# Optimization experiments

Hardware: AMD Instinct MI355X
Metric: run time of the kernel (lower is better)

The kernel has to match this reference:

```python
import jax, jax.numpy as jnp
import numpy as np

N = 2048          # target nodes
N_NODES = 2048    # neighbor pool
D_IN = 256
D_EDGE = 16
D_HID = 32
D_OUT = 256


def _mlp(h, w1, b1, w2, b2):
    # Linear -> Tanh -> Linear
    return jnp.tanh(h @ w1 + b1) @ w2 + b2


def setup_inputs() -> dict:
    key = jax.random.key(0)
    ks = jax.random.split(key, 20)
    s = 0.05
    inp = {
        "x": jax.random.normal(ks[0], (N, D_IN), jnp.float32),
        "neibs": jax.random.normal(ks[1], (N_NODES, D_IN), jnp.float32),
        "edge_emb": jax.random.normal(ks[2], (N * N_NODES, D_EDGE), jnp.float32),
        # multiplicative binary mask (float, as in original ws * mask)
        "mask": (jax.random.uniform(ks[3], (N, N_NODES)) < 0.7).astype(jnp.float32),
        "ax_w1": jax.random.normal(ks[4], (D_IN, D_HID), jnp.float32) * s,
        "ax_b1": jnp.zeros((D_HID,), jnp.float32),
        "ax_w2": jax.random.normal(ks[5], (D_HID, D_HID), jnp.float32) * s,
        "ax_b2": jnp.zeros((D_HID,), jnp.float32),
        "an_w1": jax.random.normal(ks[6], (D_IN, D_HID), jnp.float32) * s,
        "an_b1": jnp.zeros((D_HID,), jnp.float32),
        "an_w2": jax.random.normal(ks[7], (D_HID, D_HID), jnp.float32) * s,
        "an_b2": jnp.zeros((D_HID,), jnp.float32),
        "ae_w1": jax.random.normal(ks[8], (D_EDGE, D_HID), jnp.float32) * s,
        "ae_b1": jnp.zeros((D_HID,), jnp.float32),
        "ae_w2": jax.random.normal(ks[9], (D_HID, D_HID), jnp.float32) * s,
        "ae_b2": jnp.zeros((D_HID,), jnp.float32),
        "fcx_w": jax.random.normal(ks[10], (2 * D_IN, D_OUT), jnp.float32) * s,
        "fcx_b": jnp.zeros((D_OUT,), jnp.float32),
    }
    return inp


def reference(x, neibs, edge_emb, mask,
              ax_w1, ax_b1, ax_w2, ax_b2,
              an_w1, an_b1, an_w2, an_b2,
              ae_w1, ae_b1, ae_w2, ae_b2,
              fcx_w, fcx_b):
    x_att = _mlp(x, ax_w1, ax_b1, ax_w2, ax_b2)          # (N, H)
    neib_att = _mlp(neibs, an_w1, an_b1, an_w2, an_b2)   # (n_nodes, H)
    # edge attention is computed in the original forward but never used (dead code)
    _edge_att = _mlp(edge_emb, ae_w1, ae_b1, ae_w2, ae_b2)
    # multiplicative masking (NOT additive -inf), then softmax over neighbors
    ws = jnp.einsum('nh,mh->nm', x_att, neib_att) * mask  # (N, n_nodes)
    ws = jax.nn.softmax(ws, axis=1)
    agg_neib = jax.nn.sigmoid(ws @ neibs)                 # (N, D_IN)
    # concat_node=False path: concat -> fc_x -> sigmoid; dropout is identity (eval)
    out = jax.nn.sigmoid(jnp.concatenate([x, agg_neib], axis=1) @ fcx_w + fcx_b)
    return out
```

## Files before the change

### kernel.cpp

```cpp
#include <hip/hip_runtime.h>
#include <hip/hip_bf16.h>
#include <math.h>

#define NROWS 2048
#define DIN 256
#define DH 32
#define DOUT 256

typedef unsigned short ushort_t;
typedef unsigned int uint_t;

__device__ __forceinline__ float bf2f(uint_t u) {
    union { uint_t i; float f; } v; v.i = u << 16; return v.f;
}
__device__ __forceinline__ float bfhi2f(uint_t u) {
    union { uint_t i; float f; } v; v.i = u & 0xffff0000u; return v.f;
}
__device__ __forceinline__ ushort_t f2bf(float f) {
    __hip_bfloat16 h = __float2bfloat16(f);
    union { __hip_bfloat16 h; ushort_t u; } v; v.h = h; return v.u;
}
__device__ __forceinline__ float sigm(float v) { return 1.0f / (1.0f + __expf(-v)); }

__global__ __launch_bounds__(256) void mlp_kernel(
    const float* __restrict__ x, const float* __restrict__ neibs,
    const float* __restrict__ ax_w1, const float* __restrict__ ax_b1,
    const float* __restrict__ ax_w2, const float* __restrict__ ax_b2,
    const float* __restrict__ an_w1, const float* __restrict__ an_b1,
    const float* __restrict__ an_w2, const float* __restrict__ an_b2,
    float* __restrict__ x_att, ushort_t* __restrict__ n_att)
{
    const int t = threadIdx.x;
    const bool is_x = blockIdx.x < 256;
    const int row0 = (is_x ? blockIdx.x : blockIdx.x - 256) * 8;
    const float* __restrict__ in = is_x ? x : neibs;
    const float* __restrict__ w1 = is_x ? ax_w1 : an_w1;
    const float* __restrict__ b1 = is_x ? ax_b1 : an_b1;
    const float* __restrict__ w2 = is_x ? ax_w2 : an_w2;
    const float* __restrict__ b2 = is_x ? ax_b2 : an_b2;

    __shared__ float srow[8][DIN];
    __shared__ float hbuf[8][DH];

    const int r = t >> 5, c = t & 31;
    {
        const float4* in4 = (const float4*)(in + (row0 + r) * DIN);
        float4 a = in4[c * 2], b = in4[c * 2 + 1];
        *(float4*)&srow[r][c * 8] = a;
        *(float4*)&srow[r][c * 8 + 4] = b;
    }
    __syncthreads();

    float s = b1[c];
#pragma unroll 8
    for (int k = 0; k < DIN; ++k) s += srow[r][k] * w1[k * DH + c];
    s = tanhf(s);
    hbuf[r][c] = s;
    __syncthreads();

    float s2 = b2[c];
#pragma unroll
    for (int j = 0; j < DH; ++j) s2 += hbuf[r][j] * w2[j * DH + c];

    if (is_x) x_att[(row0 + r) * DH + c] = s2;
    else      n_att[(row0 + r) * DH + c] = f2bf(s2);
}

__device__ __forceinline__ void block_reduce_acc(float* red, int kc, int dg,
                                                 float (&acc)[8][8])
{
#pragma unroll
    for (int half = 4; half >= 1; half >>= 1) {
        __syncthreads();
        if (kc >= half && kc < 2 * half) {
            const int slot = kc - half;
#pragma unroll
            for (int i = 0; i < 64; ++i)
                red[slot * 2048 + i * 32 + dg] = acc[i >> 3][i & 7];
        }
        __syncthreads();
        if (kc < half) {
#pragma unroll
            for (int i = 0; i < 64; ++i)
                acc[i >> 3][i & 7] += red[kc * 2048 + i * 32 + dg];
        }
    }
}

__global__ __launch_bounds__(256) void attn_kernel(
    const float* __restrict__ x, const float* __restrict__ neibs,
    const float* __restrict__ mask,
    const float* __restrict__ x_att, const ushort_t* __restrict__ n_att,
    const float* __restrict__ fcx_w, const float* __restrict__ fcx_b,
    float* __restrict__ out)
{
    __shared__ ushort_t pT[NROWS * 8];
    __shared__ ushort_t AT[512 * 8];
    __shared__ float row_inv[8];

    const int t = threadIdx.x;
    const int n0 = blockIdx.x * 8;

    {
        uint4 q;
        uint_t pk[4];
#pragma unroll
        for (int rp = 0; rp < 4; ++rp) {
            float v0 = x[(n0 + 2 * rp) * DIN + t];
            float v1 = x[(n0 + 2 * rp + 1) * DIN + t];
            pk[rp] = (uint_t)f2bf(v0) | ((uint_t)f2bf(v1) << 16);
        }
        q.x = pk[0]; q.y = pk[1]; q.z = pk[2]; q.w = pk[3];
        *(uint4*)&AT[t * 8] = q;
    }

    const int wv = t >> 6, lane = t & 63;
    const int r0 = 2 * wv, r1 = r0 + 1;
    float xa0[DH], xa1[DH];
#pragma unroll
    for (int h = 0; h < DH; ++h) {
        xa0[h] = x_att[(n0 + r0) * DH + h];
        xa1[h] = x_att[(n0 + r1) * DH + h];
    }
    float mx0 = -1e30f, mx1 = -1e30f;
    const uint4* na4 = (const uint4*)n_att;
    for (int it = 0; it < 32; ++it) {
        const int m = it * 64 + lane;
        float s0 = 0.f, s1 = 0.f;
#pragma unroll
        for (int q = 0; q < 4; ++q) {
            uint4 v = na4[m * 4 + q];
            uint_t wsw[4] = { v.x, v.y, v.z, v.w };
#pragma unroll
            for (int u = 0; u < 4; ++u) {
                const float f0 = bf2f(wsw[u]);
                const float f1 = bfhi2f(wsw[u]);
                const int h = q * 8 + u * 2;
                s0 += xa0[h] * f0;     s1 += xa1[h] * f0;
                s0 += xa0[h + 1] * f1; s1 += xa1[h + 1] * f1;
            }
        }
        const float mk0 = mask[(n0 + r0) * NROWS + m];
        const float mk1 = mask[(n0 + r1) * NROWS + m];
        s0 *= mk0; s1 *= mk1;
        mx0 = fmaxf(mx0, s0); mx1 = fmaxf(mx1, s1);
        *(uint_t*)&pT[m * 8 + r0] = (uint_t)f2bf(s0) | ((uint_t)f2bf(s1) << 16);
    }
#pragma unroll
    for (int off = 32; off >= 1; off >>= 1) {
        mx0 = fmaxf(mx0, __shfl_xor(mx0, off));
        mx1 = fmaxf(mx1, __shfl_xor(mx1, off));
    }
    float l0 = 0.f, l1 = 0.f;
    for (int it = 0; it < 32; ++it) {
        const int m = it * 64 + lane;
        const uint_t pv = *(const uint_t*)&pT[m * 8 + r0];
        const float e0 = __expf(bf2f(pv) - mx0);
        const float e1 = __expf(bfhi2f(pv) - mx1);
        l0 += e0; l1 += e1;
        *(uint_t*)&pT[m * 8 + r0] = (uint_t)f2bf(e0) | ((uint_t)f2bf(e1) << 16);
    }
#pragma unroll
    for (int off = 32; off >= 1; off >>= 1) {
        l0 += __shfl_xor(l0, off);
        l1 += __shfl_xor(l1, off);
    }
    if (lane == 0) { row_inv[r0] = 1.f / l0; row_inv[r1] = 1.f / l1; }
    __syncthreads();

    const int kc = t >> 5, dg = t & 31, d0 = dg * 8;
    float acc[8][8];
#pragma unroll
    for (int i = 0; i < 8; ++i)
#pragma unroll
        for (int j = 0; j < 8; ++j) acc[i][j] = 0.f;

    {
        const int mbase = kc * 256;
#pragma unroll 2
        for (int mm = 0; mm < 256; ++mm) {
            const int m = mbase + mm;
            const uint4 pq = *(const uint4*)&pT[m * 8];
            float p_[8];
            p_[0] = bf2f(pq.x); p_[1] = bfhi2f(pq.x);
            p_[2] = bf2f(pq.y); p_[3] = bfhi2f(pq.y);
            p_[4] = bf2f(pq.z); p_[5] = bfhi2f(pq.z);
            p_[6] = bf2f(pq.w); p_[7] = bfhi2f(pq.w);
            const float4* nb4 = (const float4*)(neibs + m * DIN + d0);
            const float4 b0 = nb4[0], b1 = nb4[1];
#pragma unroll
            for (int r = 0; r < 8; ++r) {
                acc[r][0] += p_[r] * b0.x; acc[r][1] += p_[r] * b0.y;
                acc[r][2] += p_[r] * b0.z; acc[r][3] += p_[r] * b0.w;
                acc[r][4] += p_[r] * b1.x; acc[r][5] += p_[r] * b1.y;
                acc[r][6] += p_[r] * b1.z; acc[r][7] += p_[r] * b1.w;
            }
        }
    }

    float* red = (float*)pT;
    block_reduce_acc(red, kc, dg, acc);

    if (kc == 0) {
        float inv[8];
#pragma unroll
        for (int r2 = 0; r2 < 8; ++r2) inv[r2] = row_inv[r2];
#pragma unroll
        for (int j = 0; j < 8; ++j) {
            uint4 q;
            q.x = (uint_t)f2bf(sigm(acc[0][j] * inv[0])) | ((uint_t)f2bf(sigm(acc[1][j] * inv[1])) << 16);
            q.y = (uint_t)f2bf(sigm(acc[2][j] * inv[2])) | ((uint_t)f2bf(sigm(acc[3][j] * inv[3])) << 16);
            q.z = (uint_t)f2bf(sigm(acc[4][j] * inv[4])) | ((uint_t)f2bf(sigm(acc[5][j] * inv[5])) << 16);
            q.w = (uint_t)f2bf(sigm(acc[6][j] * inv[6])) | ((uint_t)f2bf(sigm(acc[7][j] * inv[7])) << 16);
            *(uint4*)&AT[(256 + d0 + j) * 8] = q;
        }
    }
    __syncthreads();

    float acc2[8][8];
#pragma unroll
    for (int i = 0; i < 8; ++i)
#pragma unroll
        for (int j = 0; j < 8; ++j) acc2[i][j] = 0.f;

    {
        const int kbase = kc * 64;
#pragma unroll 2
        for (int kk = 0; kk < 64; ++kk) {
            const int k = kbase + kk;
            const uint4 aq = *(const uint4*)&AT[k * 8];
            float a_[8];
            a_[0] = bf2f(aq.x); a_[1] = bfhi2f(aq.x);
            a_[2] = bf2f(aq.y); a_[3] = bfhi2f(aq.y);
            a_[4] = bf2f(aq.z); a_[5] = bfhi2f(aq.z);
            a_[6] = bf2f(aq.w); a_[7] = bfhi2f(aq.w);
            const float4* w4 = (const float4*)(fcx_w + k * DOUT + d0);
            const float4 b0 = w4[0], b1 = w4[1];
#pragma unroll
            for (int r = 0; r < 8; ++r) {
                acc2[r][0] += a_[r] * b0.x; acc2[r][1] += a_[r] * b0.y;
                acc2[r][2] += a_[r] * b0.z; acc2[r][3] += a_[r] * b0.w;
                acc2[r][4] += a_[r] * b1.x; acc2[r][5] += a_[r] * b1.y;
                acc2[r][6] += a_[r] * b1.z; acc2[r][7] += a_[r] * b1.w;
            }
        }
    }

    block_reduce_acc(red, kc, dg, acc2);

    if (kc == 0) {
        const float4 fb0 = *(const float4*)&fcx_b[d0];
        const float4 fb1 = *(const float4*)&fcx_b[d0 + 4];
        const float bia[8] = { fb0.x, fb0.y, fb0.z, fb0.w, fb1.x, fb1.y, fb1.z, fb1.w };
#pragma unroll
        for (int r2 = 0; r2 < 8; ++r2) {
            float4 o0, o1;
            o0.x = sigm(acc2[r2][0] + bia[0]); o0.y = sigm(acc2[r2][1] + bia[1]);
            o0.z = sigm(acc2[r2][2] + bia[2]); o0.w = sigm(acc2[r2][3] + bia[3]);
            o1.x = sigm(acc2[r2][4] + bia[4]); o1.y = sigm(acc2[r2][5] + bia[5]);
            o1.z = sigm(acc2[r2][6] + bia[6]); o1.w = sigm(acc2[r2][7] + bia[7]);
            *(float4*)&out[(n0 + r2) * DOUT + d0] = o0;
            *(float4*)&out[(n0 + r2) * DOUT + d0 + 4] = o1;
        }
    }
}

extern "C" void kernel_launch(void* const* d_in, const int* in_sizes, int n_in,
                              void* d_out, int out_size, void* d_ws, size_t ws_size,
                              hipStream_t stream) {
    const float* x      = (const float*)d_in[0];
    const float* neibs  = (const float*)d_in[1];
    const float* mask   = (const float*)d_in[3];
    const float* ax_w1  = (const float*)d_in[4];
    const float* ax_b1  = (const float*)d_in[5];
    const float* ax_w2  = (const float*)d_in[6];
    const float* ax_b2  = (const float*)d_in[7];
    const float* an_w1  = (const float*)d_in[8];
    const float* an_b1  = (const float*)d_in[9];
    const float* an_w2  = (const float*)d_in[10];
    const float* an_b2  = (const float*)d_in[11];
    const float* fcx_w  = (const float*)d_in[16];
    const float* fcx_b  = (const float*)d_in[17];
    float* out = (float*)d_out;

    float*    x_att = (float*)d_ws;
    ushort_t* n_att = (ushort_t*)(x_att + NROWS * DH);

    mlp_kernel<<<512, 256, 0, stream>>>(
        x, neibs, ax_w1, ax_b1, ax_w2, ax_b2,
        an_w1, an_b1, an_w2, an_b2, x_att, n_att);

    attn_kernel<<<256, 256, 0, stream>>>(
        x, neibs, mask, x_att, n_att, fcx_w, fcx_b, out);
}
```

Baseline: 444.8 us.

## Replace scalar FMA GEMMs with bf16 MFMA using prepacked neighbor and weight operands

```diff
diff --git a/kernel.cpp b/kernel.cpp
--- a/kernel.cpp
+++ b/kernel.cpp
@@ -9,12 +9,11 @@
 
 typedef unsigned short ushort_t;
 typedef unsigned int uint_t;
+typedef __attribute__((ext_vector_type(8))) short short8;
+typedef __attribute__((ext_vector_type(4))) float floatx4;
 
 __device__ __forceinline__ float bf2f(uint_t u) {
     union { uint_t i; float f; } v; v.i = u << 16; return v.f;
-}
-__device__ __forceinline__ float bfhi2f(uint_t u) {
-    union { uint_t i; float f; } v; v.i = u & 0xffff0000u; return v.f;
 }
 __device__ __forceinline__ ushort_t f2bf(float f) {
     __hip_bfloat16 h = __float2bfloat16(f);
@@ -22,99 +21,99 @@
 }
 __device__ __forceinline__ float sigm(float v) { return 1.0f / (1.0f + __expf(-v)); }
 
-__global__ __launch_bounds__(256) void mlp_kernel(
+#define PSTR 2072
+#define ASTR 536
+
+__global__ __launch_bounds__(256) void prep_kernel(
     const float* __restrict__ x, const float* __restrict__ neibs,
     const float* __restrict__ ax_w1, const float* __restrict__ ax_b1,
     const float* __restrict__ ax_w2, const float* __restrict__ ax_b2,
     const float* __restrict__ an_w1, const float* __restrict__ an_b1,
     const float* __restrict__ an_w2, const float* __restrict__ an_b2,
-    float* __restrict__ x_att, ushort_t* __restrict__ n_att)
+    const float* __restrict__ fcx_w,
+    float* __restrict__ x_att, ushort_t* __restrict__ n_att,
+    short8* __restrict__ B_pack, short8* __restrict__ W_pack)
 {
     const int t = threadIdx.x;
-    const bool is_x = blockIdx.x < 256;
-    const int row0 = (is_x ? blockIdx.x : blockIdx.x - 256) * 8;
-    const float* __restrict__ in = is_x ? x : neibs;
-    const float* __restrict__ w1 = is_x ? ax_w1 : an_w1;
-    const float* __restrict__ b1 = is_x ? ax_b1 : an_b1;
-    const float* __restrict__ w2 = is_x ? ax_w2 : an_w2;
-    const float* __restrict__ b2 = is_x ? ax_b2 : an_b2;
+    const int b = blockIdx.x;
 
     __shared__ float srow[8][DIN];
     __shared__ float hbuf[8][DH];
 
-    const int r = t >> 5, c = t & 31;
-    {
-        const float4* in4 = (const float4*)(in + (row0 + r) * DIN);
-        float4 a = in4[c * 2], b = in4[c * 2 + 1];
-        *(float4*)&srow[r][c * 8] = a;
-        *(float4*)&srow[r][c * 8 + 4] = b;
-    }
-    __syncthreads();
-
-    float s = b1[c];
+    if (b < 512) {
+        const bool is_x = b < 256;
+        const int row0 = (is_x ? b : b - 256) * 8;
+        const float* __restrict__ in = is_x ? x : neibs;
+        const float* __restrict__ w1 = is_x ? ax_w1 : an_w1;
+        const float* __restrict__ b1 = is_x ? ax_b1 : an_b1;
+        const float* __restrict__ w2 = is_x ? ax_w2 : an_w2;
+        const float* __restrict__ b2 = is_x ? ax_b2 : an_b2;
+
+        const int r = t >> 5, c = t & 31;
+        {
+            const float4* in4 = (const float4*)(in + (row0 + r) * DIN);
+            float4 a = in4[c * 2], bb = in4[c * 2 + 1];
+            *(float4*)&srow[r][c * 8] = a;
+            *(float4*)&srow[r][c * 8 + 4] = bb;
+        }
+        __syncthreads();
+
+        float s = b1[c];
 #pragma unroll 8
-    for (int k = 0; k < DIN; ++k) s += srow[r][k] * w1[k * DH + c];
-    s = tanhf(s);
-    hbuf[r][c] = s;
-    __syncthreads();
-
-    float s2 = b2[c];
-#pragma unroll
-    for (int j = 0; j < DH; ++j) s2 += hbuf[r][j] * w2[j * DH + c];
-
-    if (is_x) x_att[(row0 + r) * DH + c] = s2;
-    else      n_att[(row0 + r) * DH + c] = f2bf(s2);
-}
-
-__device__ __forceinline__ void block_reduce_acc(float* red, int kc, int dg,
-                                                 float (&acc)[8][8])
+        for (int k = 0; k < DIN; ++k) s += srow[r][k] * w1[k * DH + c];
+        s = tanhf(s);
+        hbuf[r][c] = s;
+        __syncthreads();
+
+        float s2 = b2[c];
+#pragma unroll
+        for (int j = 0; j < DH; ++j) s2 += hbuf[r][j] * w2[j * DH + c];
+
+        if (is_x) x_att[(row0 + r) * DH + c] = s2;
+        else      n_att[(row0 + r) * DH + c] = f2bf(s2);
+    } else if (b < 768) {
+        const int g = (b - 512) * 256 + t;
+        const int n = g & 15, q = (g >> 4) & 3, tt = (g >> 6) & 3, w = (g >> 8) & 3;
+        const int s = g >> 10;
+        const int ncol = w * 64 + tt * 16 + n;
+        const int kb = 32 * s + 8 * q;
+        short8 v;
+#pragma unroll
+        for (int j = 0; j < 8; ++j)
+            v[j] = (short)f2bf(neibs[(size_t)(kb + j) * DIN + ncol]);
+        B_pack[g] = v;
+    } else {
+        const int g = (b - 768) * 256 + t;
+        const int n = g & 15, q = (g >> 4) & 3, tt = (g >> 6) & 3, w = (g >> 8) & 3;
+        const int s = g >> 10;
+        const int ncol = w * 64 + tt * 16 + n;
+        const int kb = 32 * s + 8 * q;
+        short8 v;
+#pragma unroll
+        for (int j = 0; j < 8; ++j)
+            v[j] = (short)f2bf(fcx_w[(size_t)(kb + j) * DOUT + ncol]);
+        W_pack[g] = v;
+    }
+}
+
+__global__ __launch_bounds__(256) void attn_kernel(
+    const float* __restrict__ x, const float* __restrict__ mask,
+    const float* __restrict__ x_att, const ushort_t* __restrict__ n_att,
+    const short8* __restrict__ B_pack, const short8* __restrict__ W_pack,
+    const float* __restrict__ fcx_b, float* __restrict__ out)
 {
-#pragma unroll
-    for (int half = 4; half >= 1; half >>= 1) {
-        __syncthreads();
-        if (kc >= half && kc < 2 * half) {
-            const int slot = kc - half;
-#pragma unroll
-            for (int i = 0; i < 64; ++i)
-                red[slot * 2048 + i * 32 + dg] = acc[i >> 3][i & 7];
-        }
-        __syncthreads();
-        if (kc < half) {
-#pragma unroll
-            for (int i = 0; i < 64; ++i)
-                acc[i >> 3][i & 7] += red[kc * 2048 + i * 32 + dg];
-        }
-    }
-}
-
-__global__ __launch_bounds__(256) void attn_kernel(
-    const float* __restrict__ x, const float* __restrict__ neibs,
-    const float* __restrict__ mask,
-    const float* __restrict__ x_att, const ushort_t* __restrict__ n_att,
-    const float* __restrict__ fcx_w, const float* __restrict__ fcx_b,
-    float* __restrict__ out)
-{
-    __shared__ ushort_t pT[NROWS * 8];
-    __shared__ ushort_t AT[512 * 8];
+    __shared__ __align__(16) ushort_t pTr[8 * PSTR];
+    __shared__ __align__(16) ushort_t ATr[8 * ASTR];
     __shared__ float row_inv[8];
 
     const int t = threadIdx.x;
     const int n0 = blockIdx.x * 8;
-
-    {
-        uint4 q;
-        uint_t pk[4];
-#pragma unroll
-        for (int rp = 0; rp < 4; ++rp) {
-            float v0 = x[(n0 + 2 * rp) * DIN + t];
-            float v1 = x[(n0 + 2 * rp + 1) * DIN + t];
-            pk[rp] = (uint_t)f2bf(v0) | ((uint_t)f2bf(v1) << 16);
-        }
-        q.x = pk[0]; q.y = pk[1]; q.z = pk[2]; q.w = pk[3];
-        *(uint4*)&AT[t * 8] = q;
-    }
-
     const int wv = t >> 6, lane = t & 63;
+
+#pragma unroll
+    for (int r = 0; r < 8; ++r)
+        ATr[r * ASTR + t] = f2bf(x[(size_t)(n0 + r) * DIN + t]);
+
     const int r0 = 2 * wv, r1 = r0 + 1;
     float xa0[DH], xa1[DH];
 #pragma unroll
@@ -128,23 +127,23 @@
         const int m = it * 64 + lane;
         float s0 = 0.f, s1 = 0.f;
 #pragma unroll
-        for (int q = 0; q < 4; ++q) {
-            uint4 v = na4[m * 4 + q];
+        for (int qq = 0; qq < 4; ++qq) {
+            uint4 v = na4[m * 4 + qq];
             uint_t wsw[4] = { v.x, v.y, v.z, v.w };
 #pragma unroll
             for (int u = 0; u < 4; ++u) {
-                const float f0 = bf2f(wsw[u]);
-                const float f1 = bfhi2f(wsw[u]);
-                const int h = q * 8 + u * 2;
+                const float f0 = bf2f(wsw[u] & 0xffffu);
+                const float f1 = bf2f(wsw[u] >> 16);
+                const int h = qq * 8 + u * 2;
                 s0 += xa0[h] * f0;     s1 += xa1[h] * f0;
                 s0 += xa0[h + 1] * f1; s1 += xa1[h + 1] * f1;
             }
         }
-        const float mk0 = mask[(n0 + r0) * NROWS + m];
-        const float mk1 = mask[(n0 + r1) * NROWS + m];
-        s0 *= mk0; s1 *= mk1;
+        s0 *= mask[(size_t)(n0 + r0) * NROWS + m];
+        s1 *= mask[(size_t)(n0 + r1) * NROWS + m];
         mx0 = fmaxf(mx0, s0); mx1 = fmaxf(mx1, s1);
-        *(uint_t*)&pT[m * 8 + r0] = (uint_t)f2bf(s0) | ((uint_t)f2bf(s1) << 16);
+        pTr[r0 * PSTR + m] = f2bf(s0);
+        pTr[r1 * PSTR + m] = f2bf(s1);
     }
 #pragma unroll
     for (int off = 32; off >= 1; off >>= 1) {
@@ -154,11 +153,11 @@
     float l0 = 0.f, l1 = 0.f;
     for (int it = 0; it < 32; ++it) {
         const int m = it * 64 + lane;
-        const uint_t pv = *(const uint_t*)&pT[m * 8 + r0];
-        const float e0 = __expf(bf2f(pv) - mx0);
-        const float e1 = __expf(bfhi2f(pv) - mx1);
+        const float e0 = __expf(bf2f(pTr[r0 * PSTR + m]) - mx0);
+        const float e1 = __expf(bf2f(pTr[r1 * PSTR + m]) - mx1);
         l0 += e0; l1 += e1;
-        *(uint_t*)&pT[m * 8 + r0] = (uint_t)f2bf(e0) | ((uint_t)f2bf(e1) << 16);
+        pTr[r0 * PSTR + m] = f2bf(e0);
+        pTr[r1 * PSTR + m] = f2bf(e1);
     }
 #pragma unroll
     for (int off = 32; off >= 1; off >>= 1) {
@@ -168,99 +167,64 @@
     if (lane == 0) { row_inv[r0] = 1.f / l0; row_inv[r1] = 1.f / l1; }
     __syncthreads();
 
-    const int kc = t >> 5, dg = t & 31, d0 = dg * 8;
-    float acc[8][8];
-#pragma unroll
-    for (int i = 0; i < 8; ++i)
-#pragma unroll
-        for (int j = 0; j < 8; ++j) acc[i][j] = 0.f;
-
-    {
-        const int mbase = kc * 256;
-#pragma unroll 2
-        for (int mm = 0; mm < 256; ++mm) {
-            const int m = mbase + mm;
-            const uint4 pq = *(const uint4*)&pT[m * 8];
-            float p_[8];
-            p_[0] = bf2f(pq.x); p_[1] = bfhi2f(pq.x);
-            p_[2] = bf2f(pq.y); p_[3] = bfhi2f(pq.y);
-            p_[4] = bf2f(pq.z); p_[5] = bfhi2f(pq.z);
-            p_[6] = bf2f(pq.w); p_[7] = bfhi2f(pq.w);
-            const float4* nb4 = (const float4*)(neibs + m * DIN + d0);
-            const float4 b0 = nb4[0], b1 = nb4[1];
-#pragma unroll
-            for (int r = 0; r < 8; ++r) {
-                acc[r][0] += p_[r] * b0.x; acc[r][1] += p_[r] * b0.y;
-                acc[r][2] += p_[r] * b0.z; acc[r][3] += p_[r] * b0.w;
-                acc[r][4] += p_[r] * b1.x; acc[r][5] += p_[r] * b1.y;
-                acc[r][6] += p_[r] * b1.z; acc[r][7] += p_[r] * b1.w;
+    const int q = lane >> 4;
+    const int ar = lane & 7;
+    const char* aBase = (const char*)pTr + ar * (PSTR * 2) + q * 16;
+
+    floatx4 acc[4];
+#pragma unroll
+    for (int tt = 0; tt < 4; ++tt) acc[tt] = (floatx4){0.f, 0.f, 0.f, 0.f};
+
+    for (int s = 0; s < 64; ++s) {
+        const short8 av = *(const short8*)(aBase + s * 64);
+#pragma unroll
+        for (int tt = 0; tt < 4; ++tt) {
+            const int slab = (s * 4 + wv) * 4 + tt;
+            const short8 bv = B_pack[slab * 64 + lane];
+            acc[tt] = __builtin_amdgcn_mfma_f32_16x16x32_bf16(av, bv, acc[tt], 0, 0, 0);
+        }
+    }
+    if (lane < 32) {
+        const int col = lane & 15;
+        const int rbase = (lane >> 4) * 4;
+#pragma unroll
+        for (int tt = 0; tt < 4; ++tt) {
+            const int n = wv * 64 + tt * 16 + col;
+#pragma unroll
+            for (int rg = 0; rg < 4; ++rg) {
+                const int row = rbase + rg;
+                ATr[row * ASTR + 256 + n] = f2bf(sigm(acc[tt][rg] * row_inv[row]));
             }
         }
     }
-
-    float* red = (float*)pT;
-    block_reduce_acc(red, kc, dg, acc);
-
-    if (kc == 0) {
-        float inv[8];
-#pragma unroll
-        for (int r2 = 0; r2 < 8; ++r2) inv[r2] = row_inv[r2];
-#pragma unroll
-        for (int j = 0; j < 8; ++j) {
-            uint4 q;
-            q.x = (uint_t)f2bf(sigm(acc[0][j] * inv[0])) | ((uint_t)f2bf(sigm(acc[1][j] * inv[1])) << 16);
-            q.y = (uint_t)f2bf(sigm(acc[2][j] * inv[2])) | ((uint_t)f2bf(sigm(acc[3][j] * inv[3])) << 16);
-            q.z = (uint_t)f2bf(sigm(acc[4][j] * inv[4])) | ((uint_t)f2bf(sigm(acc[5][j] * inv[5])) << 16);
-            q.w = (uint_t)f2bf(sigm(acc[6][j] * inv[6])) | ((uint_t)f2bf(sigm(acc[7][j] * inv[7])) << 16);
-            *(uint4*)&AT[(256 + d0 + j) * 8] = q;
-        }
-    }
     __syncthreads();
 
-    float acc2[8][8];
-#pragma unroll
-    for (int i = 0; i < 8; ++i)
-#pragma unroll
-        for (int j = 0; j < 8; ++j) acc2[i][j] = 0.f;
-
-    {
-        const int kbase = kc * 64;
-#pragma unroll 2
-        for (int kk = 0; kk < 64; ++kk) {
-            const int k = kbase + kk;
-            const uint4 aq = *(const uint4*)&AT[k * 8];
-            float a_[8];
-            a_[0] = bf2f(aq.x); a_[1] = bfhi2f(aq.x);
-            a_[2] = bf2f(aq.y); a_[3] = bfhi2f(aq.y);
-            a_[4] = bf2f(aq.z); a_[5] = bfhi2f(aq.z);
-            a_[6] = bf2f(aq.w); a_[7] = bfhi2f(aq.w);
-            const float4* w4 = (const float4*)(fcx_w + k * DOUT + d0);
-            const float4 b0 = w4[0], b1 = w4[1];
-#pragma unroll
-            for (int r = 0; r < 8; ++r) {
-                acc2[r][0] += a_[r] * b0.x; acc2[r][1] += a_[r] * b0.y;
-                acc2[r][2] += a_[r] * b0.z; acc2[r][3] += a_[r] * b0.w;
-                acc2[r][4] += a_[r] * b1.x; acc2[r][5] += a_[r] * b1.y;
-                acc2[r][6] += a_[r] * b1.z; acc2[r][7] += a_[r] * b1.w;
+    floatx4 acc2[4];
+#pragma unroll
+    for (int tt = 0; tt < 4; ++tt) acc2[tt] = (floatx4){0.f, 0.f, 0.f, 0.f};
+
+    const char* a2Base = (const char*)ATr + ar * (ASTR * 2) + q * 16;
+    for (int s = 0; s < 16; ++s) {
+        const short8 av = *(const short8*)(a2Base + s * 64);
+#pragma unroll
+        for (int tt = 0; tt < 4; ++tt) {
+            const int slab = (s * 4 + wv) * 4 + tt;
+            const short8 bv = W_pack[slab * 64 + lane];
+            acc2[tt] = __builtin_amdgcn_mfma_f32_16x16x32_bf16(av, bv, acc2[tt], 0, 0, 0);
+        }
+    }
+    if (lane < 32) {
+        const int col = lane & 15;
+        const int rbase = (lane >> 4) * 4;
+#pragma unroll
+        for (int tt = 0; tt < 4; ++tt) {
+            const int n = wv * 64 + tt * 16 + col;
+            const float bias = fcx_b[n];
+#pragma unroll
+            for (int rg = 0; rg < 4; ++rg) {
+                const int row = rbase + rg;
+                out[(size_t)(n0 + row) * DOUT + n] = sigm(acc2[tt][rg] + bias);
             }
-        }
-    }
-
-    block_reduce_acc(red, kc, dg, acc2);
-
-    if (kc == 0) {
-        const float4 fb0 = *(const float4*)&fcx_b[d0];
-        const float4 fb1 = *(const float4*)&fcx_b[d0 + 4];
-        const float bia[8] = { fb0.x, fb0.y, fb0.z, fb0.w, fb1.x, fb1.y, fb1.z, fb1.w };
-#pragma unroll
-        for (int r2 = 0; r2 < 8; ++r2) {
-            float4 o0, o1;
-            o0.x = sigm(acc2[r2][0] + bia[0]); o0.y = sigm(acc2[r2][1] + bia[1]);
-            o0.z = sigm(acc2[r2][2] + bia[2]); o0.w = sigm(acc2[r2][3] + bia[3]);
-            o1.x = sigm(acc2[r2][4] + bia[4]); o1.y = sigm(acc2[r2][5] + bia[5]);
-            o1.z = sigm(acc2[r2][6] + bia[6]); o1.w = sigm(acc2[r2][7] + bia[7]);
-            *(float4*)&out[(n0 + r2) * DOUT + d0] = o0;
-            *(float4*)&out[(n0 + r2) * DOUT + d0 + 4] = o1;
         }
     }
 }
@@ -283,13 +247,17 @@
     const float* fcx_b  = (const float*)d_in[17];
     float* out = (float*)d_out;
 
-    float*    x_att = (float*)d_ws;
-    ushort_t* n_att = (ushort_t*)(x_att + NROWS * DH);
-
-    mlp_kernel<<<512, 256, 0, stream>>>(
+    char* ws = (char*)d_ws;
+    float*    x_att  = (float*)ws;
+    ushort_t* n_att  = (ushort_t*)(ws + 262144);
+    short8*   B_pack = (short8*)(ws + 393216);
+    short8*   W_pack = (short8*)(ws + 1441792);
+
+    prep_kernel<<<832, 256, 0, stream>>>(
         x, neibs, ax_w1, ax_b1, ax_w2, ax_b2,
-        an_w1, an_b1, an_w2, an_b2, x_att, n_att);
+        an_w1, an_b1, an_w2, an_b2, fcx_w,
+        x_att, n_att, B_pack, W_pack);
 
     attn_kernel<<<256, 256, 0, stream>>>(
-        x, neibs, mask, x_att, n_att, fcx_w, fcx_b, out);
-}
+        x, mask, x_att, n_att, B_pack, W_pack, fcx_b, out);
+}
```

Measured after the change: 411.0 us. 1.08x faster.
